# Optimization experiments

Measured on AMD Instinct MI355X. Metric: run time of the kernel, lower is better.

## Reference

```python
import jax, jax.numpy as jnp
import numpy as np

N = 50000   # nodes
E = 800000  # edges
IN, H1, H2, OUT = 128, 256, 128, 1


def setup_inputs() -> dict:
    key = jax.random.key(0)
    ks = jax.random.split(key, 9)
    x = jax.random.normal(ks[0], (N, IN), dtype=jnp.float32)
    edge_index = jax.random.randint(ks[1], (2, E), 0, N, dtype=jnp.int32)
    def glorot(k, fan_in, fan_out):
        s = np.sqrt(6.0 / (fan_in + fan_out)).astype(np.float32)
        return jax.random.uniform(k, (fan_in, fan_out), jnp.float32, -s, s)
    W1 = glorot(ks[2], IN, H1)
    b1 = jnp.zeros((H1,), jnp.float32)
    W2 = glorot(ks[3], H1, H2)
    b2 = jnp.zeros((H2,), jnp.float32)
    W3 = glorot(ks[4], H2, OUT)
    b3 = jnp.zeros((OUT,), jnp.float32)
    return {"x": x, "edge_index": edge_index, "W1": W1, "b1": b1,
            "W2": W2, "b2": b2, "W3": W3, "b3": b3}


def _gcn_layer(x, W, b, src, dst, norm):
    # dense transform [N, d_in] @ [d_in, d_out]
    h = x @ W
    # degree-normalized sparse aggregation: out[dst] += norm * h[src]
    agg = jax.ops.segment_sum(h[src] * norm[:, None], dst, num_segments=N)
    return agg + b


def reference(x, edge_index, W1, b1, W2, b2, W3, b3):
    src, dst = edge_index[0], edge_index[1]
    # PyG GCNConv: add self loops, then symmetric normalization
    loop = jnp.arange(N, dtype=src.dtype)
    src = jnp.concatenate([src, loop])
    dst = jnp.concatenate([dst, loop])
    deg = jax.ops.segment_sum(jnp.ones_like(dst, jnp.float32), dst, num_segments=N)
    dis = jax.lax.rsqrt(jnp.maximum(deg, 1.0))  # deg >= 1 via self loops
    norm = dis[src] * dis[dst]  # [E+N]
    h1 = jax.nn.relu(_gcn_layer(x, W1, b1, src, dst, norm))
    h2 = jax.nn.relu(_gcn_layer(h1, W2, b2, src, dst, norm))
    y = _gcn_layer(h2, W3, b3, src, dst, norm).reshape(-1)
    return (y, h1, h2)
```

## Files before the change

### kernel.cpp

```cpp
#include <hip/hip_runtime.h>


typedef __attribute__((ext_vector_type(8))) short short8;
typedef __attribute__((ext_vector_type(4))) float f32x4;

static __device__ __forceinline__ unsigned short f2bf(float f){
  union { float f; unsigned u; } v; v.f = f;
  unsigned r = v.u + 0x7FFF + ((v.u >> 16) & 1);
  return (unsigned short)(r >> 16);
}
static __device__ __forceinline__ float2 bf2f2(unsigned u){
  union { unsigned u; float f; } a, b;
  a.u = u << 16; b.u = u & 0xffff0000u;
  return make_float2(a.f, b.f);
}

__global__ __launch_bounds__(256) void k_prepbin(
    const int* __restrict__ src, const int* __restrict__ dst,
    int* __restrict__ bcur, unsigned* __restrict__ pairs, int E, int binB,
    const float* __restrict__ W1, const float* __restrict__ W2,
    unsigned short* __restrict__ Wf1, unsigned short* __restrict__ Wf2,
    const float4* __restrict__ x, uint2* __restrict__ xb, int nv){
  __shared__ int cl[256];
  int blk = blockIdx.x;
  int tid = threadIdx.x;
  if (blk < binB){
    int e0 = blk * 4096 + tid;
    cl[tid] = 0; __syncthreads();
    #pragma unroll
    for (int i = 0; i < 16; i++){
      int e = e0 + i*256;
      if (e < E) atomicAdd(&cl[dst[e] >> 8], 1);
    }
    __syncthreads();
    int c = cl[tid];
    int g = (c > 0) ? atomicAdd(&bcur[tid], c) : 0;
    cl[tid] = g;
    __syncthreads();
    #pragma unroll
    for (int i = 0; i < 16; i++){
      int e = e0 + i*256;
      if (e < E){
        int d = dst[e];
        int b = d >> 8;
        int p = atomicAdd(&cl[b], 1);
        pairs[(b << 13) + p] = (unsigned)src[e] | ((unsigned)(d & 255) << 16);
      }
    }
  } else if (blk < binB + 256){
    int t = (blk - binB)*256 + tid;
    if (t < 32768){
      int j = t & 7, lane = (t>>3) & 63, kt = (t>>9) & 3, nt = t >> 11;
      int nn = nt*16 + (lane & 15);
      int kk = kt*32 + (lane>>4)*8 + j;
      Wf1[t] = f2bf(W1[kk*256 + nn]);
    } else {
      int o = t - 32768;
      int j = o & 7, lane = (o>>3) & 63, ntl = (o>>9) & 3, kt = (o>>11) & 7, h = o >> 14;
      int nn = (h*4 + ntl)*16 + (lane & 15);
      int kk = kt*32 + (lane>>4)*8 + j;
      Wf2[o] = f2bf(W2[kk*128 + nn]);
    }
  } else {
    int i = (blk - binB - 256)*256 + tid;
    if (i < nv){
      float4 v = x[i];
      xb[i] = make_uint2((unsigned)f2bf(v.x) | ((unsigned)f2bf(v.y) << 16),
                         (unsigned)f2bf(v.z) | ((unsigned)f2bf(v.w) << 16));
    }
  }
}

__global__ __launch_bounds__(256) void k_place(
    const int* __restrict__ bcur, const unsigned* __restrict__ pairs,
    unsigned short* __restrict__ csr_src, int* __restrict__ rowptr,
    int* __restrict__ cnt, float* __restrict__ dis, int n, int nb){
  __shared__ int sh[256];
  __shared__ int ncnt[256];
  int t = threadIdx.x;
  int b = blockIdx.x;
  int v = (t < nb) ? bcur[t] : 0;
  sh[t] = v; __syncthreads();
  for (int off = 1; off < 256; off <<= 1){
    int x = (t >= off) ? sh[t-off] : 0;
    __syncthreads(); sh[t] += x; __syncthreads();
  }
  int csr_base = (b == 0) ? 0 : sh[b-1];
  int cnt_b = bcur[b];
  ncnt[t] = 0; __syncthreads();
  const unsigned* P = pairs + ((size_t)b << 13);
  for (int i = t; i < cnt_b; i += 256) atomicAdd(&ncnt[P[i] >> 16], 1);
  __syncthreads();
  int c = ncnt[t];
  sh[t] = c; __syncthreads();
  for (int off = 1; off < 256; off <<= 1){
    int x = (t >= off) ? sh[t-off] : 0;
    __syncthreads(); sh[t] += x; __syncthreads();
  }
  int noff = sh[t] - c;
  int node = (b << 8) + t;
  if (node < n){
    rowptr[node] = csr_base + noff;
    cnt[node] = c;
    dis[node] = rsqrtf((float)(c + 1));
  }
  ncnt[t] = noff; __syncthreads();
  for (int i = t; i < cnt_b; i += 256){
    unsigned u = P[i];
    int p = atomicAdd(&ncnt[u >> 16], 1);
    csr_src[csr_base + p] = (unsigned short)(u & 0xffff);
  }
}

__global__ void k_aggL1(const unsigned* __restrict__ xb, unsigned* __restrict__ out,
                        const int* __restrict__ rowptr, const int* __restrict__ cnt,
                        const unsigned short* __restrict__ csr_src,
                        const float* __restrict__ dis, int n){
  int t = threadIdx.x;
  int lane = t & 63;
  int node = blockIdx.x*4 + (t >> 6);
  if (node >= n) return;
  float di = dis[node];
  float2 v = bf2f2(xb[(size_t)node*64 + lane]);
  float2 acc = make_float2(di*v.x, di*v.y);
  int start = rowptr[node];
  int mm = cnt[node];
  int j = 0;
  for (; j + 15 < mm; j += 16){
    int s[16]; unsigned uv[16]; float w[16];
    #pragma unroll
    for (int q = 0; q < 16; q++) s[q] = csr_src[start+j+q];
    #pragma unroll
    for (int q = 0; q < 16; q++){ w[q] = dis[s[q]]; uv[q] = xb[(size_t)s[q]*64 + lane]; }
    #pragma unroll
    for (int q = 0; q < 16; q++){
      float2 u = bf2f2(uv[q]);
      acc.x = fmaf(w[q], u.x, acc.x); acc.y = fmaf(w[q], u.y, acc.y);
    }
  }
  for (; j + 3 < mm; j += 4){
    int s[4]; unsigned uv[4]; float w[4];
    #pragma unroll
    for (int q = 0; q < 4; q++) s[q] = csr_src[start+j+q];
    #pragma unroll
    for (int q = 0; q < 4; q++){ w[q] = dis[s[q]]; uv[q] = xb[(size_t)s[q]*64 + lane]; }
    #pragma unroll
    for (int q = 0; q < 4; q++){
      float2 u = bf2f2(uv[q]);
      acc.x = fmaf(w[q], u.x, acc.x); acc.y = fmaf(w[q], u.y, acc.y);
    }
  }
  for (; j < mm; j++){
    int s = csr_src[start+j];
    float2 u = bf2f2(xb[(size_t)s*64 + lane]);
    float w = dis[s];
    acc.x = fmaf(w, u.x, acc.x); acc.y = fmaf(w, u.y, acc.y);
  }
  acc.x *= di; acc.y *= di;
  out[(size_t)node*64 + lane] =
      (unsigned)f2bf(acc.x) | ((unsigned)f2bf(acc.y) << 16);
}

__global__ void k_aggL2(const unsigned* __restrict__ t2b, float* __restrict__ h2,
                        const int* __restrict__ rowptr, const int* __restrict__ cnt,
                        const unsigned short* __restrict__ csr_src,
                        const float* __restrict__ dis,
                        const float* __restrict__ b2, const float* __restrict__ W3,
                        float* __restrict__ u, int n){
  int t = threadIdx.x;
  int lane = t & 63;
  int node = blockIdx.x*4 + (t >> 6);
  if (node >= n) return;
  float di = dis[node];
  float2 v = bf2f2(t2b[(size_t)node*64 + lane]);
  float2 acc = make_float2(di*v.x, di*v.y);
  int start = rowptr[node];
  int mm = cnt[node];
  int j = 0;
  for (; j + 15 < mm; j += 16){
    int s[16]; unsigned uv[16]; float w[16];
    #pragma unroll
    for (int q = 0; q < 16; q++) s[q] = csr_src[start+j+q];
    #pragma unroll
    for (int q = 0; q < 16; q++){ w[q] = dis[s[q]]; uv[q] = t2b[(size_t)s[q]*64 + lane]; }
    #pragma unroll
    for (int q = 0; q < 16; q++){
      float2 uu = bf2f2(uv[q]);
      acc.x = fmaf(w[q], uu.x, acc.x); acc.y = fmaf(w[q], uu.y, acc.y);
    }
  }
  for (; j + 3 < mm; j += 4){
    int s[4]; unsigned uv[4]; float w[4];
    #pragma unroll
    for (int q = 0; q < 4; q++) s[q] = csr_src[start+j+q];
    #pragma unroll
    for (int q = 0; q < 4; q++){ w[q] = dis[s[q]]; uv[q] = t2b[(size_t)s[q]*64 + lane]; }
    #pragma unroll
    for (int q = 0; q < 4; q++){
      float2 uu = bf2f2(uv[q]);
      acc.x = fmaf(w[q], uu.x, acc.x); acc.y = fmaf(w[q], uu.y, acc.y);
    }
  }
  for (; j < mm; j++){
    int s = csr_src[start+j];
    float2 uu = bf2f2(t2b[(size_t)s*64 + lane]);
    float w = dis[s];
    acc.x = fmaf(w, uu.x, acc.x); acc.y = fmaf(w, uu.y, acc.y);
  }
  float2 b = ((const float2*)b2)[lane];
  acc.x = fmaxf(fmaf(di, acc.x, b.x), 0.0f);
  acc.y = fmaxf(fmaf(di, acc.y, b.y), 0.0f);
  ((float2*)h2)[(size_t)node*64 + lane] = acc;
  float up = fmaf(acc.x, W3[2*lane], acc.y * W3[2*lane+1]);
  #pragma unroll
  for (int off = 32; off > 0; off >>= 1) up += __shfl_down(up, off);
  if (lane == 0) u[node] = up;
}

__global__ __launch_bounds__(256) void k_gemm1_mfma(
    const unsigned short* __restrict__ Xa, const unsigned short* __restrict__ Wf1,
    const float* __restrict__ bias, float* __restrict__ out,
    unsigned short* __restrict__ h1b, int n)
{
  __shared__ unsigned short Wl[8*4*64*8];
  int t = threadIdx.x;
  int row0 = (blockIdx.x >> 1) * 64;
  int h = blockIdx.x & 1;
  int w = t >> 6, lane = t & 63, m = lane & 15, q = lane >> 4;
  int rbase = w*16;
  int rowm = row0 + rbase + m;
  int ra = (rowm < n) ? rowm : (n-1);
  const short8* Arow = (const short8*)(Xa + (size_t)ra*128);
  short8 af[4];
  #pragma unroll
  for (int kt = 0; kt < 4; kt++) af[kt] = Arow[kt*4 + q];
  {
    const float4* src = (const float4*)Wf1 + (size_t)h*2048;
    float4* dst = (float4*)Wl;
    #pragma unroll
    for (int i = 0; i < 8; i++) dst[i*256 + t] = src[i*256 + t];
  }
  __syncthreads();
  f32x4 acc[8];
  #pragma unroll
  for (int i = 0; i < 8; i++) acc[i] = (f32x4){0.f,0.f,0.f,0.f};
  const short8* Wv = (const short8*)Wl;
  #pragma unroll
  for (int nt = 0; nt < 8; nt++){
    #pragma unroll
    for (int kt = 0; kt < 4; kt++){
      short8 bfr = Wv[(nt*4 + kt)*64 + lane];
      acc[nt] = __builtin_amdgcn_mfma_f32_16x16x32_bf16(af[kt], bfr, acc[nt], 0, 0, 0);
    }
  }
  int rowa = row0 + rbase + q*4;
  int colb = h*128 + m;
  #pragma unroll
  for (int nt = 0; nt < 8; nt++){
    float b = bias[colb + nt*16];
    #pragma unroll
    for (int r = 0; r < 4; r++){
      int rr = rowa + r;
      if (rr < n){
        float o = fmaxf(acc[nt][r] + b, 0.0f);
        out[(size_t)rr*256 + colb + nt*16] = o;
        h1b[(size_t)rr*256 + colb + nt*16] = f2bf(o);
      }
    }
  }
}

__global__ __launch_bounds__(256) void k_gemm2_mfma(
    const unsigned short* __restrict__ H1b, const unsigned short* __restrict__ Wf2,
    unsigned short* __restrict__ T2b, int n)
{
  __shared__ unsigned short Wl[32*64*8];
  int t = threadIdx.x;
  int row0 = (blockIdx.x >> 1) * 64;
  int h = blockIdx.x & 1;
  int w = t >> 6, lane = t & 63, m = lane & 15, q = lane >> 4;
  int rbase = w*16;
  int rowm = row0 + rbase + m;
  int ra = (rowm < n) ? rowm : (n-1);
  const short8* Arow = (const short8*)(H1b + (size_t)ra*256);
  short8 af[8];
  #pragma unroll
  for (int kt = 0; kt < 8; kt++) af[kt] = Arow[kt*4 + q];
  {
    const float4* src = (const float4*)Wf2 + (size_t)h*2048;
    float4* dst = (float4*)Wl;
    #pragma unroll
    for (int i = 0; i < 8; i++) dst[i*256 + t] = src[i*256 + t];
  }
  __syncthreads();
  f32x4 acc[4];
  #pragma unroll
  for (int i = 0; i < 4; i++) acc[i] = (f32x4){0.f,0.f,0.f,0.f};
  const short8* Wv = (const short8*)Wl;
  #pragma unroll
  for (int nt = 0; nt < 4; nt++){
    #pragma unroll
    for (int kt = 0; kt < 8; kt++){
      short8 bfr = Wv[(kt*4 + nt)*64 + lane];
      acc[nt] = __builtin_amdgcn_mfma_f32_16x16x32_bf16(af[kt], bfr, acc[nt], 0, 0, 0);
    }
  }
  int rowa = row0 + rbase + q*4;
  #pragma unroll
  for (int nt = 0; nt < 4; nt++){
    int col = h*64 + nt*16 + m;
    #pragma unroll
    for (int r = 0; r < 4; r++){
      int rr = rowa + r;
      if (rr < n) T2b[(size_t)rr*128 + col] = f2bf(acc[nt][r]);
    }
  }
}

__global__ void k_agg1d(const float* __restrict__ u, float* __restrict__ y,
                        const int* __restrict__ rowptr, const int* __restrict__ cnt,
                        const unsigned short* __restrict__ csr_src,
                        const float* __restrict__ dis,
                        const float* __restrict__ b3, int n){
  int i = blockIdx.x*256 + threadIdx.x;
  if (i >= n) return;
  float di = dis[i];
  float acc = di * u[i];
  int s0 = rowptr[i], m = cnt[i];
  for (int j = 0; j < m; j++){
    int s = csr_src[s0+j];
    acc = fmaf(dis[s], u[s], acc);
  }
  y[i] = fmaf(di, acc, b3[0]);
}

extern "C" void kernel_launch(void* const* d_in, const int* in_sizes, int n_in,
                              void* d_out, int out_size, void* d_ws, size_t ws_size,
                              hipStream_t stream){
  const float* x  = (const float*)d_in[0];
  const int*  ei  = (const int*)d_in[1];
  const float* W1 = (const float*)d_in[2];
  const float* b1 = (const float*)d_in[3];
  const float* W2 = (const float*)d_in[4];
  const float* b2 = (const float*)d_in[5];
  const float* W3 = (const float*)d_in[6];
  const float* b3 = (const float*)d_in[7];
  const int N = in_sizes[0] / 128;
  const int E = in_sizes[1] / 2;
  const int* src = ei;
  const int* dst = ei + E;
  const int NB = (N + 255) >> 8;

  char* p = (char*)d_ws;
  auto alloc = [&](size_t bytes)->char*{
    char* r = p; p += (bytes + 255) & ~(size_t)255; return r;
  };
  int*   bcur    = (int*)  alloc(256*4);
  int*   rowptr  = (int*)  alloc((size_t)N*4);
  int*   cnt     = (int*)  alloc((size_t)N*4);
  float* dis     = (float*)alloc((size_t)N*4);
  unsigned* pairs = (unsigned*)alloc((size_t)NB*8192*4);
  unsigned short* csr_src = (unsigned short*)alloc((size_t)E*2);
  unsigned* xb   = (unsigned*)alloc((size_t)N*128*2);
  unsigned* xa   = (unsigned*)alloc((size_t)N*128*2);
  unsigned short* h1b = (unsigned short*)alloc((size_t)N*256*2);
  unsigned short* t2b = (unsigned short*)alloc((size_t)N*128*2);
  float* u       = (float*)alloc((size_t)N*4);
  unsigned short* wf1 = (unsigned short*)alloc(32768*2);
  unsigned short* wf2 = (unsigned short*)alloc(32768*2);

  float* y  = (float*)d_out;
  float* h1 = y + N;
  float* h2 = h1 + (size_t)N*256;

  int bb = (E + 4095)/4096;
  int nb = (N + 255)/256;
  int xv = N*32;
  int xblk = (xv + 255)/256;

  hipMemsetAsync(bcur, 0, 256*4, stream);
  k_prepbin <<<bb + 256 + xblk, 256, 0, stream>>>(
      src, dst, bcur, pairs, E, bb, W1, W2, wf1, wf2,
      (const float4*)x, (uint2*)xb, xv);
  k_place   <<<NB, 256, 0, stream>>>(bcur, pairs, csr_src, rowptr, cnt, dis, N, NB);

  int ab = (N + 3)/4;
  int rb = (N + 63)/64;
  k_aggL1     <<<ab,   256, 0, stream>>>(xb, xa, rowptr, cnt, csr_src, dis, N);
  k_gemm1_mfma<<<rb*2, 256, 0, stream>>>((const unsigned short*)xa, wf1, b1, h1, h1b, N);
  k_gemm2_mfma<<<rb*2, 256, 0, stream>>>(h1b, wf2, t2b, N);
  k_aggL2     <<<ab,   256, 0, stream>>>((const unsigned*)t2b, h2, rowptr, cnt, csr_src, dis, b2, W3, u, N);
  k_agg1d     <<<nb,   256, 0, stream>>>(u, y, rowptr, cnt, csr_src, dis, b3, N);
}
```

Before: 255.2 us.

## Slab-partition bf16 features into 16-column slabs for cache-local gather aggregation

Node features for both sparse aggregations are stored as 8 column slabs of 16 bf16 values (32 bytes per node per slab), written directly by the conversion and GEMM epilogue kernels. Each aggregation block handles one slab, and each wavefront processes 8 edges in parallel with 8 lanes per edge, then reduces across lanes with shuffles. The aim is to shrink each slab's working set so gathers hit in L2/MALL, and to raise memory-level parallelism per wave. In exchange there are 8x more blocks, extra shuffle reductions, and the final-layer dot product now uses atomicAdd into a zero-initialised u buffer, which needs the widened memset.

```diff
diff --git a/kernel.cpp b/kernel.cpp
--- a/kernel.cpp
+++ b/kernel.cpp
@@ -20,7 +20,7 @@
     int* __restrict__ bcur, unsigned* __restrict__ pairs, int E, int binB,
     const float* __restrict__ W1, const float* __restrict__ W2,
     unsigned short* __restrict__ Wf1, unsigned short* __restrict__ Wf2,
-    const float4* __restrict__ x, uint2* __restrict__ xb, int nv){
+    const float4* __restrict__ x, unsigned* __restrict__ xbs, int nv, int n){
   __shared__ int cl[256];
   int blk = blockIdx.x;
   int tid = threadIdx.x;
@@ -65,8 +65,11 @@
     int i = (blk - binB - 256)*256 + tid;
     if (i < nv){
       float4 v = x[i];
-      xb[i] = make_uint2((unsigned)f2bf(v.x) | ((unsigned)f2bf(v.y) << 16),
-                         (unsigned)f2bf(v.z) | ((unsigned)f2bf(v.w) << 16));
+      int row = i >> 5, c4 = i & 31;
+      int slab = c4 >> 2;
+      unsigned lo = (unsigned)f2bf(v.x) | ((unsigned)f2bf(v.y) << 16);
+      unsigned hi = (unsigned)f2bf(v.z) | ((unsigned)f2bf(v.w) << 16);
+      *(uint2*)&xbs[(size_t)slab*n*8 + row*8 + ((c4 & 3) << 1)] = make_uint2(lo, hi);
     }
   }
 }
@@ -112,113 +115,117 @@
   }
 }
 
-__global__ void k_aggL1(const unsigned* __restrict__ xb, unsigned* __restrict__ out,
+__global__ void k_aggL1(const unsigned* __restrict__ xbs, unsigned* __restrict__ xas,
                         const int* __restrict__ rowptr, const int* __restrict__ cnt,
                         const unsigned short* __restrict__ csr_src,
                         const float* __restrict__ dis, int n){
   int t = threadIdx.x;
-  int lane = t & 63;
-  int node = blockIdx.x*4 + (t >> 6);
+  int g = blockIdx.x & 7;
+  int node = (blockIdx.x >> 3)*4 + (t >> 6);
   if (node >= n) return;
+  int lane = t & 63, e = lane >> 3, c = lane & 7;
+  const unsigned* S = xbs + (size_t)g*n*8;
   float di = dis[node];
-  float2 v = bf2f2(xb[(size_t)node*64 + lane]);
-  float2 acc = make_float2(di*v.x, di*v.y);
-  int start = rowptr[node];
-  int mm = cnt[node];
+  float2 acc;
+  {
+    float2 sv = bf2f2(S[(size_t)node*8 + c]);
+    float s0 = (e == 0) ? di : 0.0f;
+    acc.x = s0*sv.x; acc.y = s0*sv.y;
+  }
+  int start = rowptr[node], mm = cnt[node];
   int j = 0;
-  for (; j + 15 < mm; j += 16){
-    int s[16]; unsigned uv[16]; float w[16];
-    #pragma unroll
-    for (int q = 0; q < 16; q++) s[q] = csr_src[start+j+q];
-    #pragma unroll
-    for (int q = 0; q < 16; q++){ w[q] = dis[s[q]]; uv[q] = xb[(size_t)s[q]*64 + lane]; }
-    #pragma unroll
-    for (int q = 0; q < 16; q++){
-      float2 u = bf2f2(uv[q]);
-      acc.x = fmaf(w[q], u.x, acc.x); acc.y = fmaf(w[q], u.y, acc.y);
-    }
-  }
-  for (; j + 3 < mm; j += 4){
-    int s[4]; unsigned uv[4]; float w[4];
-    #pragma unroll
-    for (int q = 0; q < 4; q++) s[q] = csr_src[start+j+q];
-    #pragma unroll
-    for (int q = 0; q < 4; q++){ w[q] = dis[s[q]]; uv[q] = xb[(size_t)s[q]*64 + lane]; }
+  for (; j + 31 < mm; j += 32){
+    int idx[4]; float w[4]; unsigned uv[4];
+    #pragma unroll
+    for (int q = 0; q < 4; q++) idx[q] = csr_src[start + j + q*8 + e];
+    #pragma unroll
+    for (int q = 0; q < 4; q++){ w[q] = dis[idx[q]]; uv[q] = S[(size_t)idx[q]*8 + c]; }
     #pragma unroll
     for (int q = 0; q < 4; q++){
       float2 u = bf2f2(uv[q]);
       acc.x = fmaf(w[q], u.x, acc.x); acc.y = fmaf(w[q], u.y, acc.y);
     }
   }
-  for (; j < mm; j++){
-    int s = csr_src[start+j];
-    float2 u = bf2f2(xb[(size_t)s*64 + lane]);
-    float w = dis[s];
+  for (; j < mm; j += 8){
+    int jj = j + e;
+    int idx = csr_src[start + ((jj < mm) ? jj : (mm-1))];
+    float w = (jj < mm) ? dis[idx] : 0.0f;
+    float2 u = bf2f2(S[(size_t)idx*8 + c]);
     acc.x = fmaf(w, u.x, acc.x); acc.y = fmaf(w, u.y, acc.y);
   }
-  acc.x *= di; acc.y *= di;
-  out[(size_t)node*64 + lane] =
-      (unsigned)f2bf(acc.x) | ((unsigned)f2bf(acc.y) << 16);
-}
-
-__global__ void k_aggL2(const unsigned* __restrict__ t2b, float* __restrict__ h2,
+  #pragma unroll
+  for (int off = 8; off < 64; off <<= 1){
+    acc.x += __shfl_down(acc.x, off);
+    acc.y += __shfl_down(acc.y, off);
+  }
+  if (e == 0){
+    acc.x *= di; acc.y *= di;
+    xas[(size_t)g*n*8 + (size_t)node*8 + c] =
+        (unsigned)f2bf(acc.x) | ((unsigned)f2bf(acc.y) << 16);
+  }
+}
+
+__global__ void k_aggL2(const unsigned* __restrict__ t2bs, float* __restrict__ h2,
                         const int* __restrict__ rowptr, const int* __restrict__ cnt,
                         const unsigned short* __restrict__ csr_src,
                         const float* __restrict__ dis,
                         const float* __restrict__ b2, const float* __restrict__ W3,
                         float* __restrict__ u, int n){
   int t = threadIdx.x;
-  int lane = t & 63;
-  int node = blockIdx.x*4 + (t >> 6);
+  int g = blockIdx.x & 7;
+  int node = (blockIdx.x >> 3)*4 + (t >> 6);
   if (node >= n) return;
+  int lane = t & 63, e = lane >> 3, c = lane & 7;
+  const unsigned* S = t2bs + (size_t)g*n*8;
   float di = dis[node];
-  float2 v = bf2f2(t2b[(size_t)node*64 + lane]);
-  float2 acc = make_float2(di*v.x, di*v.y);
-  int start = rowptr[node];
-  int mm = cnt[node];
+  float2 acc;
+  {
+    float2 sv = bf2f2(S[(size_t)node*8 + c]);
+    float s0 = (e == 0) ? di : 0.0f;
+    acc.x = s0*sv.x; acc.y = s0*sv.y;
+  }
+  int start = rowptr[node], mm = cnt[node];
   int j = 0;
-  for (; j + 15 < mm; j += 16){
-    int s[16]; unsigned uv[16]; float w[16];
-    #pragma unroll
-    for (int q = 0; q < 16; q++) s[q] = csr_src[start+j+q];
-    #pragma unroll
-    for (int q = 0; q < 16; q++){ w[q] = dis[s[q]]; uv[q] = t2b[(size_t)s[q]*64 + lane]; }
-    #pragma unroll
-    for (int q = 0; q < 16; q++){
-      float2 uu = bf2f2(uv[q]);
-      acc.x = fmaf(w[q], uu.x, acc.x); acc.y = fmaf(w[q], uu.y, acc.y);
-    }
-  }
-  for (; j + 3 < mm; j += 4){
-    int s[4]; unsigned uv[4]; float w[4];
-    #pragma unroll
-    for (int q = 0; q < 4; q++) s[q] = csr_src[start+j+q];
-    #pragma unroll
-    for (int q = 0; q < 4; q++){ w[q] = dis[s[q]]; uv[q] = t2b[(size_t)s[q]*64 + lane]; }
+  for (; j + 31 < mm; j += 32){
+    int idx[4]; float w[4]; unsigned uv[4];
+    #pragma unroll
+    for (int q = 0; q < 4; q++) idx[q] = csr_src[start + j + q*8 + e];
+    #pragma unroll
+    for (int q = 0; q < 4; q++){ w[q] = dis[idx[q]]; uv[q] = S[(size_t)idx[q]*8 + c]; }
     #pragma unroll
     for (int q = 0; q < 4; q++){
       float2 uu = bf2f2(uv[q]);
       acc.x = fmaf(w[q], uu.x, acc.x); acc.y = fmaf(w[q], uu.y, acc.y);
     }
   }
-  for (; j < mm; j++){
-    int s = csr_src[start+j];
-    float2 uu = bf2f2(t2b[(size_t)s*64 + lane]);
-    float w = dis[s];
+  for (; j < mm; j += 8){
+    int jj = j + e;
+    int idx = csr_src[start + ((jj < mm) ? jj : (mm-1))];
+    float w = (jj < mm) ? dis[idx] : 0.0f;
+    float2 uu = bf2f2(S[(size_t)idx*8 + c]);
     acc.x = fmaf(w, uu.x, acc.x); acc.y = fmaf(w, uu.y, acc.y);
   }
-  float2 b = ((const float2*)b2)[lane];
-  acc.x = fmaxf(fmaf(di, acc.x, b.x), 0.0f);
-  acc.y = fmaxf(fmaf(di, acc.y, b.y), 0.0f);
-  ((float2*)h2)[(size_t)node*64 + lane] = acc;
-  float up = fmaf(acc.x, W3[2*lane], acc.y * W3[2*lane+1]);
-  #pragma unroll
-  for (int off = 32; off > 0; off >>= 1) up += __shfl_down(up, off);
-  if (lane == 0) u[node] = up;
+  #pragma unroll
+  for (int off = 8; off < 64; off <<= 1){
+    acc.x += __shfl_down(acc.x, off);
+    acc.y += __shfl_down(acc.y, off);
+  }
+  if (e == 0){
+    int col = g*16 + c*2;
+    float2 b = *(const float2*)&b2[col];
+    acc.x = fmaxf(fmaf(di, acc.x, b.x), 0.0f);
+    acc.y = fmaxf(fmaf(di, acc.y, b.y), 0.0f);
+    *(float2*)&h2[(size_t)node*128 + col] = acc;
+    float up = fmaf(acc.x, W3[col], acc.y * W3[col+1]);
+    up += __shfl_down(up, 1);
+    up += __shfl_down(up, 2);
+    up += __shfl_down(up, 4);
+    if (c == 0) atomicAdd(&u[node], up);
+  }
 }
 
 __global__ __launch_bounds__(256) void k_gemm1_mfma(
-    const unsigned short* __restrict__ Xa, const unsigned short* __restrict__ Wf1,
+    const unsigned short* __restrict__ Xas, const unsigned short* __restrict__ Wf1,
     const float* __restrict__ bias, float* __restrict__ out,
     unsigned short* __restrict__ h1b, int n)
 {
@@ -230,10 +237,13 @@
   int rbase = w*16;
   int rowm = row0 + rbase + m;
   int ra = (rowm < n) ? rowm : (n-1);
-  const short8* Arow = (const short8*)(Xa + (size_t)ra*128);
+  size_t sstr = (size_t)n*16;
   short8 af[4];
   #pragma unroll
-  for (int kt = 0; kt < 4; kt++) af[kt] = Arow[kt*4 + q];
+  for (int kt = 0; kt < 4; kt++){
+    int slab = 2*kt + (q >> 1);
+    af[kt] = *(const short8*)&Xas[(size_t)slab*sstr + (size_t)ra*16 + (q & 1)*8];
+  }
   {
     const float4* src = (const float4*)Wf1 + (size_t)h*2048;
     float4* dst = (float4*)Wl;
@@ -272,7 +282,7 @@
 
 __global__ __launch_bounds__(256) void k_gemm2_mfma(
     const unsigned short* __restrict__ H1b, const unsigned short* __restrict__ Wf2,
-    unsigned short* __restrict__ T2b, int n)
+    unsigned short* __restrict__ T2s, int n)
 {
   __shared__ unsigned short Wl[32*64*8];
   int t = threadIdx.x;
@@ -305,14 +315,15 @@
       acc[nt] = __builtin_amdgcn_mfma_f32_16x16x32_bf16(af[kt], bfr, acc[nt], 0, 0, 0);
     }
   }
+  size_t sstr = (size_t)n*16;
   int rowa = row0 + rbase + q*4;
   #pragma unroll
   for (int nt = 0; nt < 4; nt++){
-    int col = h*64 + nt*16 + m;
+    int slab = h*4 + nt;
     #pragma unroll
     for (int r = 0; r < 4; r++){
       int rr = rowa + r;
-      if (rr < n) T2b[(size_t)rr*128 + col] = f2bf(acc[nt][r]);
+      if (rr < n) T2s[(size_t)slab*sstr + (size_t)rr*16 + m] = f2bf(acc[nt][r]);
     }
   }
 }
@@ -356,16 +367,16 @@
     char* r = p; p += (bytes + 255) & ~(size_t)255; return r;
   };
   int*   bcur    = (int*)  alloc(256*4);
+  float* u       = (float*)alloc((size_t)N*4);
   int*   rowptr  = (int*)  alloc((size_t)N*4);
   int*   cnt     = (int*)  alloc((size_t)N*4);
   float* dis     = (float*)alloc((size_t)N*4);
   unsigned* pairs = (unsigned*)alloc((size_t)NB*8192*4);
   unsigned short* csr_src = (unsigned short*)alloc((size_t)E*2);
-  unsigned* xb   = (unsigned*)alloc((size_t)N*128*2);
-  unsigned* xa   = (unsigned*)alloc((size_t)N*128*2);
+  unsigned* xbs  = (unsigned*)alloc((size_t)N*128*2);
+  unsigned* xas  = (unsigned*)alloc((size_t)N*128*2);
   unsigned short* h1b = (unsigned short*)alloc((size_t)N*256*2);
-  unsigned short* t2b = (unsigned short*)alloc((size_t)N*128*2);
-  float* u       = (float*)alloc((size_t)N*4);
+  unsigned short* t2s = (unsigned short*)alloc((size_t)N*128*2);
   unsigned short* wf1 = (unsigned short*)alloc(32768*2);
   unsigned short* wf2 = (unsigned short*)alloc(32768*2);
 
@@ -378,17 +389,17 @@
   int xv = N*32;
   int xblk = (xv + 255)/256;
 
-  hipMemsetAsync(bcur, 0, 256*4, stream);
+  hipMemsetAsync(bcur, 0, 256*4 + (size_t)N*4, stream);
   k_prepbin <<<bb + 256 + xblk, 256, 0, stream>>>(
       src, dst, bcur, pairs, E, bb, W1, W2, wf1, wf2,
-      (const float4*)x, (uint2*)xb, xv);
+      (const float4*)x, xbs, xv, N);
   k_place   <<<NB, 256, 0, stream>>>(bcur, pairs, csr_src, rowptr, cnt, dis, N, NB);
 
-  int ab = (N + 3)/4;
+  int ab8 = ((N + 3)/4) * 8;
   int rb = (N + 63)/64;
-  k_aggL1     <<<ab,   256, 0, stream>>>(xb, xa, rowptr, cnt, csr_src, dis, N);
-  k_gemm1_mfma<<<rb*2, 256, 0, stream>>>((const unsigned short*)xa, wf1, b1, h1, h1b, N);
-  k_gemm2_mfma<<<rb*2, 256, 0, stream>>>(h1b, wf2, t2b, N);
-  k_aggL2     <<<ab,   256, 0, stream>>>((const unsigned*)t2b, h2, rowptr, cnt, csr_src, dis, b2, W3, u, N);
+  k_aggL1     <<<ab8,  256, 0, stream>>>(xbs, xas, rowptr, cnt, csr_src, dis, N);
+  k_gemm1_mfma<<<rb*2, 256, 0, stream>>>((const unsigned short*)xas, wf1, b1, h1, h1b, N);
+  k_gemm2_mfma<<<rb*2, 256, 0, stream>>>(h1b, wf2, t2s, N);
+  k_aggL2     <<<ab8,  256, 0, stream>>>((const unsigned*)t2s, h2, rowptr, cnt, csr_src, dis, b2, W3, u, N);
   k_agg1d     <<<nb,   256, 0, stream>>>(u, y, rowptr, cnt, csr_src, dis, b3, N);
 }
```

New measurement: 485.5 us. 90.2% more time.
